# Kernel tuning notes

Hardware: AMD Instinct MI355X
Metric: run time of the kernel (lower is better)

The kernel has to match this reference:

```python
import jax, jax.numpy as jnp
import numpy as np

EPS = 1e-5  # torch InstanceNorm1d default

def _inorm(x):
    # instance norm over length dim per (batch, channel), no affine, biased var
    m = jnp.mean(x, axis=-1, keepdims=True)
    v = jnp.var(x, axis=-1, keepdims=True)
    return (x - m) * jax.lax.rsqrt(v + EPS)

def _conv1x1(W, b, x):
    # kernel-size-1 Conv1d == per-position linear: [O,C] x [B,C,T] -> [B,O,T]
    return jnp.einsum('oc,bct->bot', W, x) + b[None, :, None]

def setup_inputs() -> dict:
    key = jax.random.key(0)
    ks = jax.random.split(key, 10)
    B, C, T = 4, 512, 2048
    s = 1.0 / np.sqrt(C)  # conv1d default init scale
    return {
        'x_c': jax.random.normal(ks[0], (B, C, T), jnp.float32),
        'x_s': jax.random.normal(ks[1], (B, C, T), jnp.float32),
        'Wn': jax.random.normal(ks[2], (C, C), jnp.float32) * s,
        'bn': jax.random.normal(ks[3], (C,), jnp.float32) * s,
        'Wm': jax.random.normal(ks[4], (C, C), jnp.float32) * s,
        'bm': jax.random.normal(ks[5], (C,), jnp.float32) * s,
        'Wl': jax.random.normal(ks[6], (C, C), jnp.float32) * s,
        'bl': jax.random.normal(ks[7], (C,), jnp.float32) * s,
        'Wo': jax.random.normal(ks[8], (C, C), jnp.float32) * s,
        'bo': jax.random.normal(ks[9], (C,), jnp.float32) * s,
    }

def reference(x_c, x_s, Wn, bn, Wm, bm, Wl, bl, Wo, bo):
    Mn = _conv1x1(Wn, bn, _inorm(x_c))           # [B,C,Tc]
    Mm = _conv1x1(Wm, bm, _inorm(x_s))           # [B,C,Ts]
    A = jax.nn.softmax(jnp.einsum('bct,bcs->bts', Mn, Mm), axis=-1)  # [B,Tc,Ts]
    Ml = _conv1x1(Wl, bl, x_s)                   # [B,C,Ts]
    Mo = jnp.einsum('bcs,bts->bct', Ml, A)       # [B,C,Tc]
    return _conv1x1(Wo, bo, Mo) + x_c
```

## Files before the change

kernel.cpp:

```cpp
#include <hip/hip_runtime.h>
#include <hip/hip_bf16.h>
#include <stdint.h>

typedef _Float16 f16;
typedef _Float16 f16x8 __attribute__((ext_vector_type(8)));
typedef _Float16 f16x4 __attribute__((ext_vector_type(4)));
typedef float    f32x4 __attribute__((ext_vector_type(4)));

#define BB 4
#define CC 512
#define TT 2048

__device__ __forceinline__ void gload16(const void* g, void* l) {
  __builtin_amdgcn_global_load_lds((const __attribute__((address_space(1))) void*)g,
                                   (__attribute__((address_space(3))) void*)l, 16, 0, 0);
}

__global__ __launch_bounds__(256) void stats_kernel(
    const float* __restrict__ xc, const float* __restrict__ xs,
    float* __restrict__ meanc, float* __restrict__ invc,
    float* __restrict__ means, float* __restrict__ invs) {
  const int c = blockIdx.x, b = blockIdx.y, which = blockIdx.z;
  const float* src = (which ? xs : xc) + ((long)b * CC + c) * TT;
  const int tid = threadIdx.x;
  const float4* p4 = (const float4*)src;
  float4 a = p4[tid * 2], d = p4[tid * 2 + 1];
  float s = a.x + a.y + a.z + a.w + d.x + d.y + d.z + d.w;
  float q = a.x*a.x + a.y*a.y + a.z*a.z + a.w*a.w + d.x*d.x + d.y*d.y + d.z*d.z + d.w*d.w;
  #pragma unroll
  for (int o = 32; o; o >>= 1) { s += __shfl_xor(s, o); q += __shfl_xor(q, o); }
  __shared__ float sred[4], qred[4];
  if ((tid & 63) == 0) { sred[tid >> 6] = s; qred[tid >> 6] = q; }
  __syncthreads();
  if (tid == 0) {
    float S = sred[0] + sred[1] + sred[2] + sred[3];
    float Q = qred[0] + qred[1] + qred[2] + qred[3];
    float mean = S * (1.f / TT);
    float var  = Q * (1.f / TT) - mean * mean;
    float inv  = 1.0f / sqrtf(var + 1e-5f);
    (which ? means : meanc)[b * CC + c] = mean;
    (which ? invs  : invc )[b * CC + c] = inv;
  }
}

__global__ __launch_bounds__(256) void transpose_kernel(
    const float* __restrict__ xc, const float* __restrict__ xs,
    f16* __restrict__ xcT, f16* __restrict__ xsT) {
  const int b = blockIdx.z & 3, which = blockIdx.z >> 2;
  const float* src = (which ? xs : xc) + (long)b * CC * TT;
  f16* dst = (which ? xsT : xcT) + (long)b * TT * CC;
  const int t0 = blockIdx.x * 64, c0 = blockIdx.y * 64;
  __shared__ float tile[64][65];
  const int tid = threadIdx.x;
  #pragma unroll
  for (int it = 0; it < 4; ++it) {
    int s = it * 256 + tid, r = s >> 4, q = s & 15;
    float4 v = *(const float4*)&src[(long)(c0 + r) * TT + t0 + q * 4];
    tile[r][q*4+0] = v.x; tile[r][q*4+1] = v.y; tile[r][q*4+2] = v.z; tile[r][q*4+3] = v.w;
  }
  __syncthreads();
  #pragma unroll
  for (int it = 0; it < 4; ++it) {
    int s = it * 256 + tid, r = s >> 4, q = s & 15;
    f16x4 o;
    o[0] = (f16)tile[q*4+0][r]; o[1] = (f16)tile[q*4+1][r];
    o[2] = (f16)tile[q*4+2][r]; o[3] = (f16)tile[q*4+3][r];
    *(f16x4*)&dst[(long)(t0 + r) * CC + c0 + q * 4] = o;
  }
}

__global__ __launch_bounds__(256) void prepw_kernel(
    const float* __restrict__ W, const float* __restrict__ bias,
    const float* __restrict__ mean, const float* __restrict__ inv,
    f16* __restrict__ Weff, float* __restrict__ beff) {
  const int o = blockIdx.x, b = blockIdx.y, tid = threadIdx.x;
  float acc = 0.f;
  #pragma unroll
  for (int j = 0; j < 2; ++j) {
    int c = tid + j * 256;
    float iv = inv[b * CC + c];
    float wv = W[(long)o * CC + c] * iv;
    Weff[((long)b * CC + o) * CC + c] = (f16)wv;
    acc += wv * mean[b * CC + c];
  }
  #pragma unroll
  for (int off = 32; off; off >>= 1) acc += __shfl_xor(acc, off);
  __shared__ float red[4];
  if ((tid & 63) == 0) red[tid >> 6] = acc;
  __syncthreads();
  if (tid == 0) beff[b * CC + o] = bias[o] - (red[0] + red[1] + red[2] + red[3]);
}

__global__ __launch_bounds__(256) void f2h_kernel(const float* __restrict__ src,
                                                  f16* __restrict__ dst) {
  long i = ((long)blockIdx.x * 256 + threadIdx.x) * 8;
  float4 a = *(const float4*)&src[i], d = *(const float4*)&src[i + 4];
  f16x8 o;
  o[0]=(f16)a.x; o[1]=(f16)a.y; o[2]=(f16)a.z; o[3]=(f16)a.w;
  o[4]=(f16)d.x; o[5]=(f16)d.y; o[6]=(f16)d.z; o[7]=(f16)d.w;
  *(f16x8*)&dst[i] = o;
}

__global__ __launch_bounds__(256) void softmax_kernel(float* __restrict__ S) {
  float* p = S + ((long)blockIdx.y * TT + blockIdx.x) * TT;
  const int tid = threadIdx.x;
  float4 a = ((const float4*)p)[tid * 2], d = ((const float4*)p)[tid * 2 + 1];
  float v[8] = {a.x, a.y, a.z, a.w, d.x, d.y, d.z, d.w};
  float m = v[0];
  #pragma unroll
  for (int j = 1; j < 8; ++j) m = fmaxf(m, v[j]);
  #pragma unroll
  for (int o = 32; o; o >>= 1) m = fmaxf(m, __shfl_xor(m, o));
  __shared__ float red[4], red2[4];
  if (!(tid & 63)) red[tid >> 6] = m;
  __syncthreads();
  m = fmaxf(fmaxf(red[0], red[1]), fmaxf(red[2], red[3]));
  float e[8], sum = 0.f;
  #pragma unroll
  for (int j = 0; j < 8; ++j) { e[j] = __expf(v[j] - m); sum += e[j]; }
  #pragma unroll
  for (int o = 32; o; o >>= 1) sum += __shfl_xor(sum, o);
  if (!(tid & 63)) red2[tid >> 6] = sum;
  __syncthreads();
  sum = red2[0] + red2[1] + red2[2] + red2[3];
  float is = 1.f / sum;
  f16x8 o8;
  #pragma unroll
  for (int j = 0; j < 8; ++j) o8[j] = (f16)(e[j] * is);
  ((f16x8*)p)[tid] = o8;
}

template <typename OutT>
__device__ __forceinline__ void gemm_core(
    const f16* __restrict__ A, int lda,
    const f16* __restrict__ BT, int ldb,
    OutT* __restrict__ C, int ldc,
    const float* __restrict__ bias,
    const float* __restrict__ resid, int ldres,
    int bm, int bn, int K, bool transw) {

  __shared__ f16 sA[2][128 * 64];
  __shared__ f16 sB[2][128 * 64];

  const int tid = threadIdx.x, lane = tid & 63, wv = tid >> 6;
  const int wr = wv >> 1, wc = wv & 1;

  const int srow  = tid >> 3;
  const int scolb = (tid & 7) * 16;
  const int sgcolb = scolb ^ ((srow & 7) << 4);
  const char* gA  = (const char*)A  + (long)(bm + srow) * lda * 2 + sgcolb;
  const char* gA2 = gA + (long)64 * lda * 2;
  const char* gB  = (const char*)BT + (long)(bn + srow) * ldb * 2 + sgcolb;
  const char* gB2 = gB + (long)64 * ldb * 2;
  char* lA  = (char*)&sA[0][0] + tid * 16;
  char* lB  = (char*)&sB[0][0] + tid * 16;

  const int lm = lane & 15, lkb = (lane >> 4) * 16, sw = (lane & 7) << 4;
  int aoff[2][2], boff[4][2];
  #pragma unroll
  for (int mi = 0; mi < 2; ++mi) {
    int r = wr * 32 + mi * 16 + lm;
    #pragma unroll
    for (int kk = 0; kk < 2; ++kk)
      aoff[mi][kk] = r * 128 + ((kk * 64 + lkb) ^ sw);
  }
  #pragma unroll
  for (int ni = 0; ni < 4; ++ni) {
    int r = wc * 64 + ni * 16 + lm;
    #pragma unroll
    for (int kk = 0; kk < 2; ++kk)
      boff[ni][kk] = r * 128 + ((kk * 64 + lkb) ^ sw);
  }

  f32x4 acc[2][4] = {};
  const int nk = K >> 6;

  {
    gload16(gA, lA); gload16(gA2, lA + 8192);
    gload16(gB, lB); gload16(gB2, lB + 8192);
  }
  __syncthreads();

  int cur = 0;
  for (int kt = 0; kt < nk; ++kt) {
    if (kt + 1 < nk) {
      long kb = (long)(kt + 1) * 128;
      int nb = (cur ^ 1) * 16384;
      gload16(gA + kb, lA + nb); gload16(gA2 + kb, lA + nb + 8192);
      gload16(gB + kb, lB + nb); gload16(gB2 + kb, lB + nb + 8192);
    }
    const char* pa = (const char*)&sA[cur][0];
    const char* pb = (const char*)&sB[cur][0];
    f16x8 af[2][2], bf[4][2];
    #pragma unroll
    for (int mi = 0; mi < 2; ++mi)
      #pragma unroll
      for (int kk = 0; kk < 2; ++kk)
        af[mi][kk] = *(const f16x8*)(pa + aoff[mi][kk]);
    #pragma unroll
    for (int ni = 0; ni < 4; ++ni)
      #pragma unroll
      for (int kk = 0; kk < 2; ++kk)
        bf[ni][kk] = *(const f16x8*)(pb + boff[ni][kk]);
    #pragma unroll
    for (int kk = 0; kk < 2; ++kk)
      #pragma unroll
      for (int mi = 0; mi < 2; ++mi)
        #pragma unroll
        for (int ni = 0; ni < 4; ++ni)
          acc[mi][ni] = __builtin_amdgcn_mfma_f32_16x16x32_f16(af[mi][kk], bf[ni][kk], acc[mi][ni], 0, 0, 0);
    __syncthreads();
    cur ^= 1;
  }

  struct alignas(4 * sizeof(OutT)) Pack4 { OutT v[4]; };
  const int rr = (lane >> 4) * 4;
  #pragma unroll
  for (int mi = 0; mi < 2; ++mi) {
    int m0 = bm + wr * 32 + mi * 16 + rr;
    #pragma unroll
    for (int ni = 0; ni < 4; ++ni) {
      int n0 = bn + wc * 64 + ni * 16 + lm;
      f32x4 v = acc[mi][ni];
      float vals[4];
      #pragma unroll
      for (int r = 0; r < 4; ++r) {
        vals[r] = v[r];
        if (bias)  vals[r] += bias[m0 + r];
        if (resid) vals[r] += resid[(long)(m0 + r) * ldres + n0];
      }
      if (transw) {
        Pack4 pk;
        #pragma unroll
        for (int r = 0; r < 4; ++r) pk.v[r] = (OutT)vals[r];
        *(Pack4*)&C[(long)n0 * ldc + m0] = pk;
      } else {
        #pragma unroll
        for (int r = 0; r < 4; ++r)
          C[(long)(m0 + r) * ldc + n0] = (OutT)vals[r];
      }
    }
  }
}

__global__ __launch_bounds__(512) void conv_kernel(
    const f16* __restrict__ xcT, const f16* __restrict__ xsT,
    const f16* __restrict__ WnE, const float* __restrict__ bnE,
    const f16* __restrict__ WmE, const float* __restrict__ bmE,
    const f16* __restrict__ WlB, const float* __restrict__ bl,
    f16* __restrict__ MnT, f16* __restrict__ MmT, f16* __restrict__ Ml) {
  const int z = blockIdx.z, cid = z >> 2, b = z & 3;
  const f16* A; const float* bias; const f16* B; f16* C; int ldc; bool transw;
  if (cid == 0)      { A = WnE + (long)b*CC*CC; bias = bnE + b*CC; B = xcT + (long)b*TT*CC; C = MnT + (long)b*TT*CC; ldc = CC; transw = true; }
  else if (cid == 1) { A = WmE + (long)b*CC*CC; bias = bmE + b*CC; B = xsT + (long)b*TT*CC; C = MmT + (long)b*TT*CC; ldc = CC; transw = true; }
  else               { A = WlB;                 bias = bl;         B = xsT + (long)b*TT*CC; C = Ml  + (long)b*CC*TT; ldc = TT; transw = false; }
  gemm_core<f16>(A, CC, B, CC, C, ldc, bias, nullptr, 0,
                 blockIdx.y * 128, blockIdx.x * 128, CC, transw);
}

__global__ __launch_bounds__(512) void sgemm_kernel(
    const f16* __restrict__ MnT, const f16* __restrict__ MmT, float* __restrict__ S) {
  const int b = blockIdx.z;
  gemm_core<float>(MnT + (long)b*TT*CC, CC, MmT + (long)b*TT*CC, CC,
                   S + (long)b*TT*TT, TT, nullptr, nullptr, 0,
                   blockIdx.y * 128, blockIdx.x * 128, CC, false);
}

__global__ __launch_bounds__(512) void pv_kernel(
    const f16* __restrict__ P, const f16* __restrict__ Ml, f16* __restrict__ MoT) {
  const int b = blockIdx.z;
  gemm_core<f16>(P + (long)b*TT*2*TT, 2*TT, Ml + (long)b*CC*TT, TT,
                 MoT + (long)b*TT*CC, CC, nullptr, nullptr, 0,
                 blockIdx.y * 128, blockIdx.x * 128, TT, false);
}

__global__ __launch_bounds__(512) void out_kernel(
    const f16* __restrict__ WoB, const f16* __restrict__ MoT,
    const float* __restrict__ bo, const float* __restrict__ xc, float* __restrict__ out) {
  const int b = blockIdx.z;
  gemm_core<float>(WoB, CC, MoT + (long)b*TT*CC, CC,
                   out + (long)b*CC*TT, TT, bo, xc + (long)b*CC*TT, TT,
                   blockIdx.y * 128, blockIdx.x * 128, CC, false);
}

extern "C" void kernel_launch(void* const* d_in, const int* in_sizes, int n_in,
                              void* d_out, int out_size, void* d_ws, size_t ws_size,
                              hipStream_t stream) {
  const float* x_c = (const float*)d_in[0];
  const float* x_s = (const float*)d_in[1];
  const float* Wn  = (const float*)d_in[2];
  const float* bn  = (const float*)d_in[3];
  const float* Wm  = (const float*)d_in[4];
  const float* bm  = (const float*)d_in[5];
  const float* Wl  = (const float*)d_in[6];
  const float* bl  = (const float*)d_in[7];
  const float* Wo  = (const float*)d_in[8];
  const float* bo  = (const float*)d_in[9];
  float* out = (float*)d_out;

  char* w = (char*)d_ws;
  auto alloc = [&](size_t bytes) { char* p = w; w += (bytes + 255) & ~(size_t)255; return p; };
  float* meanc = (float*)alloc(BB * CC * 4);
  float* invc  = (float*)alloc(BB * CC * 4);
  float* means = (float*)alloc(BB * CC * 4);
  float* invs  = (float*)alloc(BB * CC * 4);
  float* bnE   = (float*)alloc(BB * CC * 4);
  float* bmE   = (float*)alloc(BB * CC * 4);
  f16* WnE = (f16*)alloc((size_t)BB * CC * CC * 2);
  f16* WmE = (f16*)alloc((size_t)BB * CC * CC * 2);
  f16* WlB = (f16*)alloc((size_t)CC * CC * 2);
  f16* WoB = (f16*)alloc((size_t)CC * CC * 2);
  f16* xcT = (f16*)alloc((size_t)BB * TT * CC * 2);
  f16* xsT = (f16*)alloc((size_t)BB * TT * CC * 2);
  f16* MnT = (f16*)alloc((size_t)BB * TT * CC * 2);
  f16* MmT = (f16*)alloc((size_t)BB * TT * CC * 2);
  f16* Ml  = (f16*)alloc((size_t)BB * CC * TT * 2);
  float* S  = (float*)alloc((size_t)BB * TT * TT * 4);
  f16* MoT = (f16*)alloc((size_t)BB * TT * CC * 2);

  stats_kernel<<<dim3(CC, BB, 2), dim3(256), 0, stream>>>(x_c, x_s, meanc, invc, means, invs);
  transpose_kernel<<<dim3(TT / 64, CC / 64, BB * 2), dim3(256), 0, stream>>>(x_c, x_s, xcT, xsT);
  prepw_kernel<<<dim3(CC, BB), dim3(256), 0, stream>>>(Wn, bn, meanc, invc, WnE, bnE);
  prepw_kernel<<<dim3(CC, BB), dim3(256), 0, stream>>>(Wm, bm, means, invs, WmE, bmE);
  f2h_kernel<<<dim3(CC * CC / (256 * 8)), dim3(256), 0, stream>>>(Wl, WlB);
  f2h_kernel<<<dim3(CC * CC / (256 * 8)), dim3(256), 0, stream>>>(Wo, WoB);

  conv_kernel<<<dim3(16, 4, 12), dim3(512), 0, stream>>>(
      xcT, xsT, WnE, bnE, WmE, bmE, WlB, bl, MnT, MmT, Ml);
  sgemm_kernel<<<dim3(16, 16, BB), dim3(512), 0, stream>>>(MnT, MmT, S);
  softmax_kernel<<<dim3(TT, BB), dim3(256), 0, stream>>>(S);
  pv_kernel<<<dim3(4, 16, BB), dim3(512), 0, stream>>>((const f16*)S, Ml, MoT);
  out_kernel<<<dim3(16, 4, BB), dim3(512), 0, stream>>>(WoB, MoT, bo, x_c, out);
}
```

Measured before the change: 239.5 us.

## Fuse stats into transpose, store scores in fp16, retile PV/out GEMMs, add XCD swizzle

Folds the instance-norm statistics into the transpose kernel using atomics, so one pass over the inputs and one launch are removed. The score matrix is now written as fp16 instead of fp32, halving the traffic of the sgemm, softmax and PV stages. The GEMM core is templated on tile height and thread count, so PV and the output projection run with smaller 64-row tiles, 256 threads and more blocks. All GEMM kernels also remap block IDs to spread neighbouring tiles across XCDs. Risks are fp16 score range and precision, and atomic contention on the channel sums.

```diff
diff --git a/kernel.cpp b/kernel.cpp
--- a/kernel.cpp
+++ b/kernel.cpp
@@ -16,39 +16,24 @@
                                    (__attribute__((address_space(3))) void*)l, 16, 0, 0);
 }
 
-__global__ __launch_bounds__(256) void stats_kernel(
-    const float* __restrict__ xc, const float* __restrict__ xs,
-    float* __restrict__ meanc, float* __restrict__ invc,
-    float* __restrict__ means, float* __restrict__ invs) {
-  const int c = blockIdx.x, b = blockIdx.y, which = blockIdx.z;
-  const float* src = (which ? xs : xc) + ((long)b * CC + c) * TT;
-  const int tid = threadIdx.x;
-  const float4* p4 = (const float4*)src;
-  float4 a = p4[tid * 2], d = p4[tid * 2 + 1];
-  float s = a.x + a.y + a.z + a.w + d.x + d.y + d.z + d.w;
-  float q = a.x*a.x + a.y*a.y + a.z*a.z + a.w*a.w + d.x*d.x + d.y*d.y + d.z*d.z + d.w*d.w;
-  #pragma unroll
-  for (int o = 32; o; o >>= 1) { s += __shfl_xor(s, o); q += __shfl_xor(q, o); }
-  __shared__ float sred[4], qred[4];
-  if ((tid & 63) == 0) { sred[tid >> 6] = s; qred[tid >> 6] = q; }
-  __syncthreads();
-  if (tid == 0) {
-    float S = sred[0] + sred[1] + sred[2] + sred[3];
-    float Q = qred[0] + qred[1] + qred[2] + qred[3];
-    float mean = S * (1.f / TT);
-    float var  = Q * (1.f / TT) - mean * mean;
-    float inv  = 1.0f / sqrtf(var + 1e-5f);
-    (which ? means : meanc)[b * CC + c] = mean;
-    (which ? invs  : invc )[b * CC + c] = inv;
-  }
+__device__ __forceinline__ void xcd_swizzle(int& bx, int& by, int& bz) {
+  int gx = gridDim.x, gy = gridDim.y;
+  int F = bx + gx * (by + gy * bz);
+  int q = (gx * gy * gridDim.z) >> 3;
+  int l = (F & 7) * q + (F >> 3);
+  bx = l % gx; by = (l / gx) % gy; bz = l / (gx * gy);
 }
 
 __global__ __launch_bounds__(256) void transpose_kernel(
     const float* __restrict__ xc, const float* __restrict__ xs,
-    f16* __restrict__ xcT, f16* __restrict__ xsT) {
+    f16* __restrict__ xcT, f16* __restrict__ xsT,
+    float* __restrict__ sumc, float* __restrict__ sqc,
+    float* __restrict__ sums_, float* __restrict__ sqs) {
   const int b = blockIdx.z & 3, which = blockIdx.z >> 2;
   const float* src = (which ? xs : xc) + (long)b * CC * TT;
   f16* dst = (which ? xsT : xcT) + (long)b * TT * CC;
+  float* sumP = (which ? sums_ : sumc) + b * CC;
+  float* sqP  = (which ? sqs   : sqc ) + b * CC;
   const int t0 = blockIdx.x * 64, c0 = blockIdx.y * 64;
   __shared__ float tile[64][65];
   const int tid = threadIdx.x;
@@ -57,6 +42,14 @@
     int s = it * 256 + tid, r = s >> 4, q = s & 15;
     float4 v = *(const float4*)&src[(long)(c0 + r) * TT + t0 + q * 4];
     tile[r][q*4+0] = v.x; tile[r][q*4+1] = v.y; tile[r][q*4+2] = v.z; tile[r][q*4+3] = v.w;
+    float ps = v.x + v.y + v.z + v.w;
+    float pq = v.x*v.x + v.y*v.y + v.z*v.z + v.w*v.w;
+    #pragma unroll
+    for (int o = 8; o; o >>= 1) { ps += __shfl_xor(ps, o); pq += __shfl_xor(pq, o); }
+    if ((tid & 15) == 0) {
+      atomicAdd(&sumP[c0 + r], ps);
+      atomicAdd(&sqP [c0 + r], pq);
+    }
   }
   __syncthreads();
   #pragma unroll
@@ -71,17 +64,19 @@
 
 __global__ __launch_bounds__(256) void prepw_kernel(
     const float* __restrict__ W, const float* __restrict__ bias,
-    const float* __restrict__ mean, const float* __restrict__ inv,
+    const float* __restrict__ sum, const float* __restrict__ sq,
     f16* __restrict__ Weff, float* __restrict__ beff) {
   const int o = blockIdx.x, b = blockIdx.y, tid = threadIdx.x;
   float acc = 0.f;
   #pragma unroll
   for (int j = 0; j < 2; ++j) {
     int c = tid + j * 256;
-    float iv = inv[b * CC + c];
+    float mean = sum[b * CC + c] * (1.f / TT);
+    float var  = sq [b * CC + c] * (1.f / TT) - mean * mean;
+    float iv = 1.0f / sqrtf(var + 1e-5f);
     float wv = W[(long)o * CC + c] * iv;
     Weff[((long)b * CC + o) * CC + c] = (f16)wv;
-    acc += wv * mean[b * CC + c];
+    acc += wv * mean;
   }
   #pragma unroll
   for (int off = 32; off; off >>= 1) acc += __shfl_xor(acc, off);
@@ -101,11 +96,13 @@
   *(f16x8*)&dst[i] = o;
 }
 
-__global__ __launch_bounds__(256) void softmax_kernel(float* __restrict__ S) {
-  float* p = S + ((long)blockIdx.y * TT + blockIdx.x) * TT;
+__global__ __launch_bounds__(256) void softmax_kernel(f16* __restrict__ S) {
+  f16* p = S + ((long)blockIdx.y * TT + blockIdx.x) * TT;
   const int tid = threadIdx.x;
-  float4 a = ((const float4*)p)[tid * 2], d = ((const float4*)p)[tid * 2 + 1];
-  float v[8] = {a.x, a.y, a.z, a.w, d.x, d.y, d.z, d.w};
+  f16x8 v8 = ((const f16x8*)p)[tid];
+  float v[8];
+  #pragma unroll
+  for (int j = 0; j < 8; ++j) v[j] = (float)v8[j];
   float m = v[0];
   #pragma unroll
   for (int j = 1; j < 8; ++j) m = fmaxf(m, v[j]);
@@ -130,7 +127,7 @@
   ((f16x8*)p)[tid] = o8;
 }
 
-template <typename OutT>
+template <int BM, int NT, typename OutT>
 __device__ __forceinline__ void gemm_core(
     const f16* __restrict__ A, int lda,
     const f16* __restrict__ BT, int ldb,
@@ -139,21 +136,33 @@
     const float* __restrict__ resid, int ldres,
     int bm, int bn, int K, bool transw) {
 
-  __shared__ f16 sA[2][128 * 64];
-  __shared__ f16 sB[2][128 * 64];
+  constexpr int CA = BM * 8 / NT;
+  constexpr int CB = 128 * 8 / NT;
+  constexpr int ABUFB = BM * 128;
+  constexpr int BBUFB = 128 * 128;
+
+  __shared__ f16 sA[2 * BM * 64];
+  __shared__ f16 sB[2 * 128 * 64];
 
   const int tid = threadIdx.x, lane = tid & 63, wv = tid >> 6;
   const int wr = wv >> 1, wc = wv & 1;
 
-  const int srow  = tid >> 3;
-  const int scolb = (tid & 7) * 16;
-  const int sgcolb = scolb ^ ((srow & 7) << 4);
-  const char* gA  = (const char*)A  + (long)(bm + srow) * lda * 2 + sgcolb;
-  const char* gA2 = gA + (long)64 * lda * 2;
-  const char* gB  = (const char*)BT + (long)(bn + srow) * ldb * 2 + sgcolb;
-  const char* gB2 = gB + (long)64 * ldb * 2;
-  char* lA  = (char*)&sA[0][0] + tid * 16;
-  char* lB  = (char*)&sB[0][0] + tid * 16;
+  const char* gAp[CA]; int lAo[CA];
+  #pragma unroll
+  for (int i = 0; i < CA; ++i) {
+    int cid = tid + i * NT, row = cid >> 3;
+    int colb = ((cid & 7) * 16) ^ ((row & 7) << 4);
+    gAp[i] = (const char*)A + (long)(bm + row) * lda * 2 + colb;
+    lAo[i] = cid * 16;
+  }
+  const char* gBp[CB]; int lBo[CB];
+  #pragma unroll
+  for (int i = 0; i < CB; ++i) {
+    int cid = tid + i * NT, row = cid >> 3;
+    int colb = ((cid & 7) * 16) ^ ((row & 7) << 4);
+    gBp[i] = (const char*)BT + (long)(bn + row) * ldb * 2 + colb;
+    lBo[i] = cid * 16;
+  }
 
   const int lm = lane & 15, lkb = (lane >> 4) * 16, sw = (lane & 7) << 4;
   int aoff[2][2], boff[4][2];
@@ -175,22 +184,24 @@
   f32x4 acc[2][4] = {};
   const int nk = K >> 6;
 
-  {
-    gload16(gA, lA); gload16(gA2, lA + 8192);
-    gload16(gB, lB); gload16(gB2, lB + 8192);
-  }
+  #pragma unroll
+  for (int i = 0; i < CA; ++i) gload16(gAp[i], (char*)sA + lAo[i]);
+  #pragma unroll
+  for (int i = 0; i < CB; ++i) gload16(gBp[i], (char*)sB + lBo[i]);
   __syncthreads();
 
   int cur = 0;
   for (int kt = 0; kt < nk; ++kt) {
     if (kt + 1 < nk) {
       long kb = (long)(kt + 1) * 128;
-      int nb = (cur ^ 1) * 16384;
-      gload16(gA + kb, lA + nb); gload16(gA2 + kb, lA + nb + 8192);
-      gload16(gB + kb, lB + nb); gload16(gB2 + kb, lB + nb + 8192);
+      int na = (cur ^ 1) * ABUFB, nb = (cur ^ 1) * BBUFB;
+      #pragma unroll
+      for (int i = 0; i < CA; ++i) gload16(gAp[i] + kb, (char*)sA + na + lAo[i]);
+      #pragma unroll
+      for (int i = 0; i < CB; ++i) gload16(gBp[i] + kb, (char*)sB + nb + lBo[i]);
     }
-    const char* pa = (const char*)&sA[cur][0];
-    const char* pb = (const char*)&sB[cur][0];
+    const char* pa = (const char*)sA + cur * ABUFB;
+    const char* pb = (const char*)sB + cur * BBUFB;
     f16x8 af[2][2], bf[4][2];
     #pragma unroll
     for (int mi = 0; mi < 2; ++mi)
@@ -249,38 +260,43 @@
     const f16* __restrict__ WmE, const float* __restrict__ bmE,
     const f16* __restrict__ WlB, const float* __restrict__ bl,
     f16* __restrict__ MnT, f16* __restrict__ MmT, f16* __restrict__ Ml) {
-  const int z = blockIdx.z, cid = z >> 2, b = z & 3;
+  int bx = blockIdx.x, by = blockIdx.y, bz = blockIdx.z;
+  xcd_swizzle(bx, by, bz);
+  const int cid = bz >> 2, b = bz & 3;
   const f16* A; const float* bias; const f16* B; f16* C; int ldc; bool transw;
   if (cid == 0)      { A = WnE + (long)b*CC*CC; bias = bnE + b*CC; B = xcT + (long)b*TT*CC; C = MnT + (long)b*TT*CC; ldc = CC; transw = true; }
   else if (cid == 1) { A = WmE + (long)b*CC*CC; bias = bmE + b*CC; B = xsT + (long)b*TT*CC; C = MmT + (long)b*TT*CC; ldc = CC; transw = true; }
   else               { A = WlB;                 bias = bl;         B = xsT + (long)b*TT*CC; C = Ml  + (long)b*CC*TT; ldc = TT; transw = false; }
-  gemm_core<f16>(A, CC, B, CC, C, ldc, bias, nullptr, 0,
-                 blockIdx.y * 128, blockIdx.x * 128, CC, transw);
+  gemm_core<128, 512, f16>(A, CC, B, CC, C, ldc, bias, nullptr, 0,
+                           by * 128, bx * 128, CC, transw);
 }
 
 __global__ __launch_bounds__(512) void sgemm_kernel(
-    const f16* __restrict__ MnT, const f16* __restrict__ MmT, float* __restrict__ S) {
-  const int b = blockIdx.z;
-  gemm_core<float>(MnT + (long)b*TT*CC, CC, MmT + (long)b*TT*CC, CC,
-                   S + (long)b*TT*TT, TT, nullptr, nullptr, 0,
-                   blockIdx.y * 128, blockIdx.x * 128, CC, false);
-}
-
-__global__ __launch_bounds__(512) void pv_kernel(
+    const f16* __restrict__ MnT, const f16* __restrict__ MmT, f16* __restrict__ S) {
+  int bx = blockIdx.x, by = blockIdx.y, bz = blockIdx.z;
+  xcd_swizzle(bx, by, bz);
+  gemm_core<128, 512, f16>(MnT + (long)bz*TT*CC, CC, MmT + (long)bz*TT*CC, CC,
+                           S + (long)bz*TT*TT, TT, nullptr, nullptr, 0,
+                           by * 128, bx * 128, CC, false);
+}
+
+__global__ __launch_bounds__(256) void pv_kernel(
     const f16* __restrict__ P, const f16* __restrict__ Ml, f16* __restrict__ MoT) {
-  const int b = blockIdx.z;
-  gemm_core<f16>(P + (long)b*TT*2*TT, 2*TT, Ml + (long)b*CC*TT, TT,
-                 MoT + (long)b*TT*CC, CC, nullptr, nullptr, 0,
-                 blockIdx.y * 128, blockIdx.x * 128, TT, false);
-}
-
-__global__ __launch_bounds__(512) void out_kernel(
+  int bx = blockIdx.x, by = blockIdx.y, bz = blockIdx.z;
+  xcd_swizzle(bx, by, bz);
+  gemm_core<64, 256, f16>(P + (long)bz*TT*TT, TT, Ml + (long)bz*CC*TT, TT,
+                          MoT + (long)bz*TT*CC, CC, nullptr, nullptr, 0,
+                          by * 64, bx * 128, TT, false);
+}
+
+__global__ __launch_bounds__(256) void out_kernel(
     const f16* __restrict__ WoB, const f16* __restrict__ MoT,
     const float* __restrict__ bo, const float* __restrict__ xc, float* __restrict__ out) {
-  const int b = blockIdx.z;
-  gemm_core<float>(WoB, CC, MoT + (long)b*TT*CC, CC,
-                   out + (long)b*CC*TT, TT, bo, xc + (long)b*CC*TT, TT,
-                   blockIdx.y * 128, blockIdx.x * 128, CC, false);
+  int bx = blockIdx.x, by = blockIdx.y, bz = blockIdx.z;
+  xcd_swizzle(bx, by, bz);
+  gemm_core<64, 256, float>(WoB, CC, MoT + (long)bz*TT*CC, CC,
+                            out + (long)bz*CC*TT, TT, bo, xc + (long)bz*CC*TT, TT,
+                            by * 64, bx * 128, CC, false);
 }
 
 extern "C" void kernel_launch(void* const* d_in, const int* in_sizes, int n_in,
@@ -300,12 +316,12 @@
 
   char* w = (char*)d_ws;
   auto alloc = [&](size_t bytes) { char* p = w; w += (bytes + 255) & ~(size_t)255; return p; };
-  float* meanc = (float*)alloc(BB * CC * 4);
-  float* invc  = (float*)alloc(BB * CC * 4);
-  float* means = (float*)alloc(BB * CC * 4);
-  float* invs  = (float*)alloc(BB * CC * 4);
-  float* bnE   = (float*)alloc(BB * CC * 4);
-  float* bmE   = (float*)alloc(BB * CC * 4);
+  float* sumc = (float*)alloc(BB * CC * 4);
+  float* sqc  = (float*)alloc(BB * CC * 4);
+  float* sums_ = (float*)alloc(BB * CC * 4);
+  float* sqs  = (float*)alloc(BB * CC * 4);
+  float* bnE  = (float*)alloc(BB * CC * 4);
+  float* bmE  = (float*)alloc(BB * CC * 4);
   f16* WnE = (f16*)alloc((size_t)BB * CC * CC * 2);
   f16* WmE = (f16*)alloc((size_t)BB * CC * CC * 2);
   f16* WlB = (f16*)alloc((size_t)CC * CC * 2);
@@ -315,13 +331,15 @@
   f16* MnT = (f16*)alloc((size_t)BB * TT * CC * 2);
   f16* MmT = (f16*)alloc((size_t)BB * TT * CC * 2);
   f16* Ml  = (f16*)alloc((size_t)BB * CC * TT * 2);
-  float* S  = (float*)alloc((size_t)BB * TT * TT * 4);
+  f16* S   = (f16*)alloc((size_t)BB * TT * TT * 2);
   f16* MoT = (f16*)alloc((size_t)BB * TT * CC * 2);
 
-  stats_kernel<<<dim3(CC, BB, 2), dim3(256), 0, stream>>>(x_c, x_s, meanc, invc, means, invs);
-  transpose_kernel<<<dim3(TT / 64, CC / 64, BB * 2), dim3(256), 0, stream>>>(x_c, x_s, xcT, xsT);
-  prepw_kernel<<<dim3(CC, BB), dim3(256), 0, stream>>>(Wn, bn, meanc, invc, WnE, bnE);
-  prepw_kernel<<<dim3(CC, BB), dim3(256), 0, stream>>>(Wm, bm, means, invs, WmE, bmE);
+  hipMemsetAsync(sumc, 0, (size_t)4 * BB * CC * 4, stream);
+
+  transpose_kernel<<<dim3(TT / 64, CC / 64, BB * 2), dim3(256), 0, stream>>>(
+      x_c, x_s, xcT, xsT, sumc, sqc, sums_, sqs);
+  prepw_kernel<<<dim3(CC, BB), dim3(256), 0, stream>>>(Wn, bn, sumc, sqc, WnE, bnE);
+  prepw_kernel<<<dim3(CC, BB), dim3(256), 0, stream>>>(Wm, bm, sums_, sqs, WmE, bmE);
   f2h_kernel<<<dim3(CC * CC / (256 * 8)), dim3(256), 0, stream>>>(Wl, WlB);
   f2h_kernel<<<dim3(CC * CC / (256 * 8)), dim3(256), 0, stream>>>(Wo, WoB);
 
@@ -329,6 +347,6 @@
       xcT, xsT, WnE, bnE, WmE, bmE, WlB, bl, MnT, MmT, Ml);
   sgemm_kernel<<<dim3(16, 16, BB), dim3(512), 0, stream>>>(MnT, MmT, S);
   softmax_kernel<<<dim3(TT, BB), dim3(256), 0, stream>>>(S);
-  pv_kernel<<<dim3(4, 16, BB), dim3(512), 0, stream>>>((const f16*)S, Ml, MoT);
-  out_kernel<<<dim3(16, 4, BB), dim3(512), 0, stream>>>(WoB, MoT, bo, x_c, out);
-}
+  pv_kernel<<<dim3(4, 32, BB), dim3(256), 0, stream>>>(S, Ml, MoT);
+  out_kernel<<<dim3(16, 8, BB), dim3(256), 0, stream>>>(WoB, MoT, bo, x_c, out);
+}
```

After: 234.8 us. 1.02x faster.
